# Kernel optimization log

Hardware: AMD Instinct MI355X
Metric: run time of the kernel (lower is better)

The kernel has to match this reference:

```python
import jax, jax.numpy as jnp
import numpy as np

B, D, H, W, Q = 16, 768, 64, 64, 128


def setup_inputs() -> dict:
    key = jax.random.key(0)
    ks = jax.random.split(key, 6)
    s = 0.02  # param init scale
    return {
        "visual_feat": jax.random.normal(ks[0], (B, D, H, W), jnp.float32),
        "text_feat": jax.random.normal(ks[1], (B, Q, D), jnp.float32),
        "Wq": jax.random.normal(ks[2], (D, D), jnp.float32) * s,
        "bq": jnp.zeros((D,), jnp.float32),
        "Wk": jax.random.normal(ks[3], (D, D), jnp.float32) * s,
        "bk": jnp.zeros((D,), jnp.float32),
        "Wv": jax.random.normal(ks[4], (D, D), jnp.float32) * s,
        "bv": jnp.zeros((D,), jnp.float32),
    }


def _entropy_weights(x):
    # x: [B, T, D] -> softmax over features, per-token entropy, softmax over tokens -> [B, T]
    p = jax.nn.softmax(x, axis=-1)
    ent = -jnp.sum(p * jnp.log(p + 1e-9), axis=-1)
    return jax.nn.softmax(ent, axis=-1)


def reference(visual_feat, text_feat, Wq, bq, Wk, bk, Wv, bv):
    b, d, h, w = visual_feat.shape
    vf = visual_feat.reshape(b, d, h * w).transpose(0, 2, 1)  # [B, N, D]
    ve = _entropy_weights(vf)          # [B, N]
    te = _entropy_weights(text_feat)   # [B, Q]
    q = vf @ Wq.T + bq                 # [B, N, D]
    k = text_feat @ Wk.T + bk          # [B, Q, D]
    v = text_feat @ Wv.T + bv          # [B, Q, D]
    attn = jnp.einsum('bnd,bqd->bnq', q, k) / jnp.sqrt(jnp.float32(d))
    attn = attn * (ve[:, :, None] * te[:, None, :])  # entropy outer-product modulation
    attn = jax.nn.softmax(attn, axis=-1)
    enhanced = jnp.einsum('bnq,bqd->bnd', attn, v)   # [B, N, D]
    return enhanced.transpose(0, 2, 1).reshape(b, d, h, w)
```

## Files before the change

kernel.cpp:

```cpp
#include <hip/hip_runtime.h>

#define B_ 16
#define D_ 768
#define N_ 4096
#define Q_ 128

typedef __attribute__((ext_vector_type(4))) float f32x4;
typedef __attribute__((ext_vector_type(8))) short short8;
typedef __attribute__((ext_vector_type(4))) short sv4;

__device__ __forceinline__ unsigned short f2bf(float f) {
  union { float f; unsigned u; } x; x.f = f;
  unsigned u = x.u;
  unsigned r = u + 0x7fffu + ((u >> 16) & 1u);
  return (unsigned short)(r >> 16);
}
__device__ __forceinline__ float bf2f(unsigned short h) {
  union { unsigned u; float f; } x; x.u = ((unsigned)h) << 16;
  return x.f;
}

__global__ __launch_bounds__(256) void cast_bf16_kernel(
    const float* __restrict__ src, unsigned short* __restrict__ dst, int n4) {
  int i = blockIdx.x * 256 + threadIdx.x;
  if (i >= n4) return;
  float4 v = ((const float4*)src)[i];
  ushort4 o;
  o.x = f2bf(v.x); o.y = f2bf(v.y); o.z = f2bf(v.z); o.w = f2bf(v.w);
  ((ushort4*)dst)[i] = o;
}

__global__ __launch_bounds__(256) void transpose_cast_kernel(
    const float* __restrict__ src, unsigned short* __restrict__ dst, int rows, int cols) {
  __shared__ float tile[32][33];
  int bx = blockIdx.x * 32, by = blockIdx.y * 32;
  int tx = threadIdx.x & 31, ty = threadIdx.x >> 5;
  #pragma unroll
  for (int i = 0; i < 32; i += 8)
    tile[ty + i][tx] = src[(size_t)(by + ty + i) * cols + bx + tx];
  __syncthreads();
  #pragma unroll
  for (int i = 0; i < 32; i += 8)
    dst[(size_t)(bx + ty + i) * rows + by + tx] = f2bf(tile[tx][ty + i]);
}

__global__ __launch_bounds__(256) void row_entropy_kernel(
    const float* __restrict__ X, float* __restrict__ ent, int K) {
  int row = blockIdx.x * 4 + (threadIdx.x >> 6);
  int lane = threadIdx.x & 63;
  const float* x = X + (size_t)row * K;
  float m = -__builtin_inff(), s = 0.f, t = 0.f;
  for (int k = lane; k < K; k += 64) {
    float v = x[k];
    float nm = fmaxf(m, v);
    float c = __expf(m - nm);
    float e = __expf(v - nm);
    s = s * c + e;
    t = t * c + v * e;
    m = nm;
  }
  #pragma unroll
  for (int off = 32; off > 0; off >>= 1) {
    float m2 = __shfl_xor(m, off);
    float s2 = __shfl_xor(s, off);
    float t2 = __shfl_xor(t, off);
    float nm = fmaxf(m, m2);
    float c1 = __expf(m - nm), c2 = __expf(m2 - nm);
    s = s * c1 + s2 * c2;
    t = t * c1 + t2 * c2;
    m = nm;
  }
  if (lane == 0) ent[row] = m + __logf(s) - t / s;
}

__global__ __launch_bounds__(256) void visual_entropy_kernel(
    const float* __restrict__ vis, float* __restrict__ ent) {
  int bb = blockIdx.x >> 6;
  int n0 = (blockIdx.x & 63) * 64;
  int t = threadIdx.x;
  int tok = t & 63;
  int slice = t >> 6;
  const float* base = vis + (size_t)bb * D_ * N_ + (size_t)slice * 192 * N_ + n0 + tok;
  float m = -__builtin_inff(), s = 0.f, tt = 0.f;
  for (int d = 0; d < 192; d++) {
    float v = base[(size_t)d * N_];
    float nm = fmaxf(m, v);
    float c = __expf(m - nm);
    float e = __expf(v - nm);
    s = s * c + e; tt = tt * c + v * e; m = nm;
  }
  __shared__ float sm[256], ss[256], st[256];
  sm[t] = m; ss[t] = s; st[t] = tt;
  __syncthreads();
  if (t < 64) {
    #pragma unroll
    for (int k = 1; k < 4; k++) {
      float m2 = sm[t + 64 * k], s2 = ss[t + 64 * k], t2 = st[t + 64 * k];
      float nm = fmaxf(m, m2);
      float c1 = __expf(m - nm), c2 = __expf(m2 - nm);
      s = s * c1 + s2 * c2; tt = tt * c1 + t2 * c2; m = nm;
    }
    ent[(size_t)bb * N_ + n0 + t] = m + __logf(s) - tt / s;
  }
}

__global__ __launch_bounds__(128) void softmax128_kernel(
    const float* __restrict__ ent, float* __restrict__ w) {
  int b = blockIdx.x, t = threadIdx.x;
  float v = ent[b * 128 + t];
  float m = v;
  #pragma unroll
  for (int off = 32; off; off >>= 1) m = fmaxf(m, __shfl_xor(m, off));
  __shared__ float sm2[2], ssum[2];
  int wv = t >> 6;
  if ((t & 63) == 0) sm2[wv] = m;
  __syncthreads();
  m = fmaxf(sm2[0], sm2[1]);
  float e = __expf(v - m);
  float s = e;
  #pragma unroll
  for (int off = 32; off; off >>= 1) s += __shfl_xor(s, off);
  if ((t & 63) == 0) ssum[wv] = s;
  __syncthreads();
  s = ssum[0] + ssum[1];
  w[b * 128 + t] = e / s;
}

__global__ __launch_bounds__(1024) void softmax4096_kernel(
    const float* __restrict__ ent, float* __restrict__ w) {
  int b = blockIdx.x, t = threadIdx.x;
  const float* e = ent + (size_t)b * N_;
  float v[4];
  float m = -__builtin_inff();
  #pragma unroll
  for (int i = 0; i < 4; i++) { v[i] = e[t + 1024 * i]; m = fmaxf(m, v[i]); }
  #pragma unroll
  for (int off = 32; off; off >>= 1) m = fmaxf(m, __shfl_xor(m, off));
  __shared__ float red[16];
  int wv = t >> 6;
  if ((t & 63) == 0) red[wv] = m;
  __syncthreads();
  if (t < 16) {
    float x = red[t];
    #pragma unroll
    for (int off = 8; off; off >>= 1) x = fmaxf(x, __shfl_xor(x, off));
    red[t] = x;
  }
  __syncthreads();
  m = red[0];
  float ev[4];
  float s = 0.f;
  #pragma unroll
  for (int i = 0; i < 4; i++) { ev[i] = __expf(v[i] - m); s += ev[i]; }
  #pragma unroll
  for (int off = 32; off; off >>= 1) s += __shfl_xor(s, off);
  __syncthreads();
  if ((t & 63) == 0) red[wv] = s;
  __syncthreads();
  if (t < 16) {
    float x = red[t];
    #pragma unroll
    for (int off = 8; off; off >>= 1) x += __shfl_xor(x, off);
    red[t] = x;
  }
  __syncthreads();
  s = red[0];
  #pragma unroll
  for (int i = 0; i < 4; i++) w[(size_t)b * N_ + t + 1024 * i] = ev[i] / s;
}

template <int MODE>
__global__ __launch_bounds__(256) void gemm_nt_kernel(
    const unsigned short* __restrict__ A, const unsigned short* __restrict__ Bm,
    const float* __restrict__ bias, unsigned short* __restrict__ C) {
  constexpr int LDA = 40;
  __shared__ unsigned short As[64 * LDA];
  __shared__ unsigned short Bs[64 * LDA];
  int m0 = blockIdx.x * 64, n0 = blockIdx.y * 64;
  int t = threadIdx.x, wave = t >> 6, lane = t & 63;
  int wm = (wave & 1) * 32, wn = (wave >> 1) * 32;
  int fl = lane & 15, fq = lane >> 4;
  f32x4 acc[2][2];
  #pragma unroll
  for (int i = 0; i < 2; i++)
    #pragma unroll
    for (int j = 0; j < 2; j++) acc[i][j] = {0.f, 0.f, 0.f, 0.f};
  int sr = t >> 2, sc = (t & 3) * 8;
  for (int k0 = 0; k0 < D_; k0 += 32) {
    uint4 av = *(const uint4*)(A + (size_t)(m0 + sr) * D_ + k0 + sc);
    uint4 bv = *(const uint4*)(Bm + (size_t)(n0 + sr) * D_ + k0 + sc);
    __syncthreads();
    *(uint4*)(As + sr * LDA + sc) = av;
    *(uint4*)(Bs + sr * LDA + sc) = bv;
    __syncthreads();
    short8 afr[2], bfr[2];
    #pragma unroll
    for (int i = 0; i < 2; i++)
      afr[i] = *(const short8*)(As + (wm + i * 16 + fl) * LDA + fq * 8);
    #pragma unroll
    for (int j = 0; j < 2; j++)
      bfr[j] = *(const short8*)(Bs + (wn + j * 16 + fl) * LDA + fq * 8);
    #pragma unroll
    for (int i = 0; i < 2; i++)
      #pragma unroll
      for (int j = 0; j < 2; j++)
        acc[i][j] = __builtin_amdgcn_mfma_f32_16x16x32_bf16(afr[i], bfr[j], acc[i][j], 0, 0, 0);
  }
  #pragma unroll
  for (int i = 0; i < 2; i++)
    #pragma unroll
    for (int j = 0; j < 2; j++) {
      int n = n0 + wn + j * 16 + fl;
      float bb = (MODE >= 1) ? bias[n] : 0.f;
      #pragma unroll
      for (int r = 0; r < 4; r++) {
        int m = m0 + wm + i * 16 + fq * 4 + r;
        float val = acc[i][j][r] + bb;
        if (MODE == 2) {
          int bt = m >> 7, q = m & 127;
          C[((size_t)bt * D_ + n) * Q_ + q] = f2bf(val);
        } else {
          C[(size_t)m * D_ + n] = f2bf(val);
        }
      }
    }
}

__global__ __launch_bounds__(256) void bias_dot_kernel(
    const unsigned short* __restrict__ kb, const float* __restrict__ bq,
    float* __restrict__ skq) {
  int row = blockIdx.x * 4 + (threadIdx.x >> 6);
  int lane = threadIdx.x & 63;
  const unsigned short* kr = kb + (size_t)row * D_;
  float s = 0.f;
  for (int k = lane; k < D_; k += 64) s += bq[k] * bf2f(kr[k]);
  #pragma unroll
  for (int off = 32; off; off >>= 1) s += __shfl_xor(s, off);
  if (lane == 0) skq[row] = s;
}

__global__ __launch_bounds__(256, 2) void attn_main_kernel(
    const float* __restrict__ vis,
    const unsigned short* __restrict__ kq,
    const unsigned short* __restrict__ vT,
    const float* __restrict__ ve,
    const float* __restrict__ te,
    const float* __restrict__ skq,
    float* __restrict__ out)
{
  constexpr int LA = 68;
  constexpr int LB = 72;
  constexpr int LP = 136;
  __shared__ unsigned short region0[30464];
  __shared__ float stats[2][128][2];
  unsigned short* As = region0;
  unsigned short* Bs = region0 + 8704;
  unsigned short* Ps = region0;
  unsigned short* Vs = region0 + 17408;

  const int bb = blockIdx.x >> 5;
  const int n0 = (blockIdx.x & 31) * 128;
  const int t = threadIdx.x;
  const int wave = t >> 6, lane = t & 63;
  const int fl = lane & 15, fq = lane >> 4;
  const int wm = (wave & 1) * 64;
  const int wq = (wave >> 1) * 64;

  const float* abase = vis + (size_t)bb * D_ * N_ + n0;
  const unsigned short* bbase = kq + (size_t)bb * Q_ * D_;

  f32x4 acc[4][4];
  #pragma unroll
  for (int i = 0; i < 4; i++)
    #pragma unroll
    for (int j = 0; j < 4; j++) acc[i][j] = {0.f, 0.f, 0.f, 0.f};

  const int smi = t & 127;
  const int ph = t >> 7;

  for (int k0 = 0; k0 < D_; k0 += 64) {
    __syncthreads();
    #pragma unroll
    for (int i = 0; i < 16; i++) {
      const int kk = 2 * (ph + 2 * i);
      const float v0 = abase[(size_t)(k0 + kk) * N_ + smi];
      const float v1 = abase[(size_t)(k0 + kk + 1) * N_ + smi];
      const unsigned pk = (unsigned)f2bf(v0) | ((unsigned)f2bf(v1) << 16);
      *(unsigned*)(As + smi * LA + kk) = pk;
    }
    #pragma unroll
    for (int i = 0; i < 4; i++) {
      const int c = t + 256 * i;
      const int q = c >> 3, kc = (c & 7) * 8;
      const uint4 v = *(const uint4*)(bbase + (size_t)q * D_ + k0 + kc);
      *(uint4*)(Bs + q * LB + kc) = v;
    }
    __syncthreads();
    #pragma unroll
    for (int ks = 0; ks < 2; ks++) {
      short8 afr[4], bfr[4];
      #pragma unroll
      for (int i = 0; i < 4; i++) {
        const unsigned short* pa = As + (wm + i * 16 + fl) * LA + ks * 32 + fq * 8;
        sv4 lo = *(const sv4*)pa;
        sv4 hi = *(const sv4*)(pa + 4);
        afr[i] = __builtin_shufflevector(lo, hi, 0, 1, 2, 3, 4, 5, 6, 7);
      }
      #pragma unroll
      for (int j = 0; j < 4; j++)
        bfr[j] = *(const short8*)(Bs + (wq + j * 16 + fl) * LB + ks * 32 + fq * 8);
      #pragma unroll
      for (int i = 0; i < 4; i++)
        #pragma unroll
        for (int j = 0; j < 4; j++)
          acc[i][j] = __builtin_amdgcn_mfma_f32_16x16x32_bf16(afr[i], bfr[j], acc[i][j], 0, 0, 0);
    }
  }

  const float rsD = 0.03608439182435161f;
  float tev[4], skv[4];
  #pragma unroll
  for (int j = 0; j < 4; j++) {
    int q = wq + j * 16 + fl;
    tev[j] = te[bb * Q_ + q];
    skv[j] = skq[bb * Q_ + q];
  }
  float vev4[4][4];
  #pragma unroll
  for (int i = 0; i < 4; i++)
    #pragma unroll
    for (int r = 0; r < 4; r++)
      vev4[i][r] = ve[(size_t)bb * N_ + n0 + wm + i * 16 + fq * 4 + r];

  float rmax[4][4], rsum[4][4];
  #pragma unroll
  for (int i = 0; i < 4; i++)
    #pragma unroll
    for (int r = 0; r < 4; r++) rmax[i][r] = -__builtin_inff();
  #pragma unroll
  for (int i = 0; i < 4; i++)
    #pragma unroll
    for (int j = 0; j < 4; j++)
      #pragma unroll
      for (int r = 0; r < 4; r++) {
        float L = (acc[i][j][r] + skv[j]) * rsD * vev4[i][r] * tev[j];
        acc[i][j][r] = L;
        rmax[i][r] = fmaxf(rmax[i][r], L);
      }
  #pragma unroll
  for (int off = 1; off < 16; off <<= 1)
    #pragma unroll
    for (int i = 0; i < 4; i++)
      #pragma unroll
      for (int r = 0; r < 4; r++)
        rmax[i][r] = fmaxf(rmax[i][r], __shfl_xor(rmax[i][r], off));
  #pragma unroll
  for (int i = 0; i < 4; i++)
    #pragma unroll
    for (int r = 0; r < 4; r++) rsum[i][r] = 0.f;
  #pragma unroll
  for (int i = 0; i < 4; i++)
    #pragma unroll
    for (int j = 0; j < 4; j++)
      #pragma unroll
      for (int r = 0; r < 4; r++) {
        float e = __expf(acc[i][j][r] - rmax[i][r]);
        acc[i][j][r] = e;
        rsum[i][r] += e;
      }
  #pragma unroll
  for (int off = 1; off < 16; off <<= 1)
    #pragma unroll
    for (int i = 0; i < 4; i++)
      #pragma unroll
      for (int r = 0; r < 4; r++) rsum[i][r] += __shfl_xor(rsum[i][r], off);

  const int qh = wq >> 6;
  if (fl == 0) {
    #pragma unroll
    for (int i = 0; i < 4; i++)
      #pragma unroll
      for (int r = 0; r < 4; r++) {
        int m = wm + i * 16 + fq * 4 + r;
        stats[qh][m][0] = rmax[i][r];
        stats[qh][m][1] = rsum[i][r];
      }
  }
  __syncthreads();
  float fac[4][4];
  #pragma unroll
  for (int i = 0; i < 4; i++)
    #pragma unroll
    for (int r = 0; r < 4; r++) {
      int m = wm + i * 16 + fq * 4 + r;
      float M2 = stats[1 - qh][m][0], S2 = stats[1 - qh][m][1];
      float Mf = fmaxf(rmax[i][r], M2);
      float sf = rsum[i][r] * __expf(rmax[i][r] - Mf) + S2 * __expf(M2 - Mf);
      fac[i][r] = __expf(rmax[i][r] - Mf) / sf;
    }
  #pragma unroll
  for (int i = 0; i < 4; i++)
    #pragma unroll
    for (int j = 0; j < 4; j++)
      #pragma unroll
      for (int r = 0; r < 4; r++) {
        int m = wm + i * 16 + fq * 4 + r;
        int q = wq + j * 16 + fl;
        Ps[m * LP + q] = f2bf(acc[i][j][r] * fac[i][r]);
      }

  const int wd = (wave & 1) * 48;
  const int wm2 = (wave >> 1) * 64;
  for (int dc = 0; dc < 8; dc++) {
    __syncthreads();
    const unsigned short* vbase = vT + ((size_t)bb * D_ + dc * 96) * Q_;
    #pragma unroll
    for (int i = 0; i < 6; i++) {
      const int c = t + 256 * i;
      const int d = c >> 4, qc = (c & 15) * 8;
      const uint4 v = *(const uint4*)(vbase + (size_t)d * Q_ + qc);
      *(uint4*)(Vs + d * LP + qc) = v;
    }
    __syncthreads();
    f32x4 acc2[3][4];
    #pragma unroll
    for (int i = 0; i < 3; i++)
      #pragma unroll
      for (int j = 0; j < 4; j++) acc2[i][j] = {0.f, 0.f, 0.f, 0.f};
    #pragma unroll
    for (int ks = 0; ks < 4; ks++) {
      short8 vfr[3], pfr[4];
      #pragma unroll
      for (int i = 0; i < 3; i++)
        vfr[i] = *(const short8*)(Vs + (wd + i * 16 + fl) * LP + ks * 32 + fq * 8);
      #pragma unroll
      for (int j = 0; j < 4; j++)
        pfr[j] = *(const short8*)(Ps + (wm2 + j * 16 + fl) * LP + ks * 32 + fq * 8);
      #pragma unroll
      for (int i = 0; i < 3; i++)
        #pragma unroll
        for (int j = 0; j < 4; j++)
          acc2[i][j] = __builtin_amdgcn_mfma_f32_16x16x32_bf16(vfr[i], pfr[j], acc2[i][j], 0, 0, 0);
    }
    float* obase = out + ((size_t)bb * D_ + dc * 96) * N_ + n0;
    #pragma unroll
    for (int i = 0; i < 3; i++)
      #pragma unroll
      for (int j = 0; j < 4; j++) {
        int mm = wm2 + j * 16 + fl;
        #pragma unroll
        for (int r = 0; r < 4; r++) {
          int d = wd + i * 16 + fq * 4 + r;
          obase[(size_t)d * N_ + mm] = acc2[i][j][r];
        }
      }
  }
}

extern "C" void kernel_launch(void* const* d_in, const int* in_sizes, int n_in,
                              void* d_out, int out_size, void* d_ws, size_t ws_size,
                              hipStream_t stream) {
  const float* vis  = (const float*)d_in[0];
  const float* text = (const float*)d_in[1];
  const float* Wq   = (const float*)d_in[2];
  const float* bq   = (const float*)d_in[3];
  const float* Wk   = (const float*)d_in[4];
  const float* bk   = (const float*)d_in[5];
  const float* Wv   = (const float*)d_in[6];
  const float* bv   = (const float*)d_in[7];
  float* out = (float*)d_out;
  char* ws = (char*)d_ws;

  unsigned short* textb = (unsigned short*)(ws + 0);
  unsigned short* Wkb   = (unsigned short*)(ws + 3145728);
  unsigned short* Wvb   = (unsigned short*)(ws + 4325376);
  unsigned short* WqTb  = (unsigned short*)(ws + 5505024);
  unsigned short* kb    = (unsigned short*)(ws + 6684672);
  unsigned short* kqb   = (unsigned short*)(ws + 9830400);
  unsigned short* vTb   = (unsigned short*)(ws + 12976128);
  float* ent_t = (float*)(ws + 16121856);
  float* tew   = (float*)(ws + 16130048);
  float* ent_v = (float*)(ws + 16138240);
  float* vew   = (float*)(ws + 16400384);
  float* skq   = (float*)(ws + 16662528);

  cast_bf16_kernel<<<1536, 256, 0, stream>>>(text, textb, 2048 * 768 / 4);
  cast_bf16_kernel<<<576, 256, 0, stream>>>(Wk, Wkb, 768 * 768 / 4);
  cast_bf16_kernel<<<576, 256, 0, stream>>>(Wv, Wvb, 768 * 768 / 4);
  transpose_cast_kernel<<<dim3(24, 24), 256, 0, stream>>>(Wq, WqTb, 768, 768);

  row_entropy_kernel<<<512, 256, 0, stream>>>(text, ent_t, 768);
  softmax128_kernel<<<16, 128, 0, stream>>>(ent_t, tew);
  visual_entropy_kernel<<<1024, 256, 0, stream>>>(vis, ent_v);
  softmax4096_kernel<<<16, 1024, 0, stream>>>(ent_v, vew);

  gemm_nt_kernel<1><<<dim3(32, 12), 256, 0, stream>>>(textb, Wkb, bk, kb);
  gemm_nt_kernel<2><<<dim3(32, 12), 256, 0, stream>>>(textb, Wvb, bv, vTb);
  gemm_nt_kernel<0><<<dim3(32, 12), 256, 0, stream>>>(kb, WqTb, nullptr, kqb);
  bias_dot_kernel<<<512, 256, 0, stream>>>(kb, bq, skq);

  attn_main_kernel<<<512, 256, 0, stream>>>(vis, kqb, vTb, vew, tew, skq, out);
}
```

Before: 463.9 us.

## Fuse visual bf16 transpose into entropy pass and async-load attention tiles

The visual entropy kernel now also writes a token-major bf16 copy of the visual features, so the attention kernel can load A tiles with direct global-to-LDS async copies into a swizzled layout instead of doing strided fp32 loads and converting per block. The K·Wq product is reassociated to precompute Wq^T·Wk once, with bias terms folded into vectors u, bw and c0, which removes the dependent k GEMM. This adds roughly 100 MB of extra bf16 write and read traffic, traded against removing the repeated fp32 conversion inside the main kernel.

```diff
diff --git a/kernel.cpp b/kernel.cpp
--- a/kernel.cpp
+++ b/kernel.cpp
@@ -15,9 +15,11 @@
   unsigned r = u + 0x7fffu + ((u >> 16) & 1u);
   return (unsigned short)(r >> 16);
 }
-__device__ __forceinline__ float bf2f(unsigned short h) {
-  union { unsigned u; float f; } x; x.u = ((unsigned)h) << 16;
-  return x.f;
+
+__device__ __forceinline__ void async16(unsigned short* lds, const unsigned short* g) {
+  __builtin_amdgcn_global_load_lds(
+      (const __attribute__((address_space(1))) unsigned int*)g,
+      (__attribute__((address_space(3))) unsigned int*)lds, 16, 0, 0);
 }
 
 __global__ __launch_bounds__(256) void cast_bf16_kernel(
@@ -73,23 +75,38 @@
   if (lane == 0) ent[row] = m + __logf(s) - t / s;
 }
 
-__global__ __launch_bounds__(256) void visual_entropy_kernel(
-    const float* __restrict__ vis, float* __restrict__ ent) {
+__global__ __launch_bounds__(256) void visual_fused_kernel(
+    const float* __restrict__ vis, unsigned short* __restrict__ vfT,
+    float* __restrict__ ent) {
+  constexpr int LT = 72;
+  __shared__ unsigned short tile[64 * LT];
+  __shared__ float sm[256], ss[256], st[256];
   int bb = blockIdx.x >> 6;
   int n0 = (blockIdx.x & 63) * 64;
-  int t = threadIdx.x;
-  int tok = t & 63;
-  int slice = t >> 6;
-  const float* base = vis + (size_t)bb * D_ * N_ + (size_t)slice * 192 * N_ + n0 + tok;
+  int t = threadIdx.x, tok = t & 63, j = t >> 6;
+  const float* base = vis + (size_t)bb * D_ * N_ + n0 + tok;
+  unsigned short* orow = vfT + (size_t)(bb * N_ + n0) * D_;
   float m = -__builtin_inff(), s = 0.f, tt = 0.f;
-  for (int d = 0; d < 192; d++) {
-    float v = base[(size_t)d * N_];
-    float nm = fmaxf(m, v);
-    float c = __expf(m - nm);
-    float e = __expf(v - nm);
-    s = s * c + e; tt = tt * c + v * e; m = nm;
-  }
-  __shared__ float sm[256], ss[256], st[256];
+  for (int dc = 0; dc < 12; dc++) {
+    __syncthreads();
+    #pragma unroll
+    for (int i = 0; i < 16; i++) {
+      int dl = j * 16 + i;
+      float v = base[(size_t)(dc * 64 + dl) * N_];
+      float nm = fmaxf(m, v);
+      float c = __expf(m - nm), e = __expf(v - nm);
+      s = s * c + e; tt = tt * c + v * e; m = nm;
+      tile[tok * LT + dl] = f2bf(v);
+    }
+    __syncthreads();
+    #pragma unroll
+    for (int i2 = 0; i2 < 2; i2++) {
+      int V = i2 * 256 + t;
+      int r = V >> 3, cv = V & 7;
+      short8 pk = *(const short8*)(tile + r * LT + cv * 8);
+      *(short8*)(orow + (size_t)r * D_ + dc * 64 + cv * 8) = pk;
+    }
+  }
   sm[t] = m; ss[t] = s; st[t] = tt;
   __syncthreads();
   if (t < 64) {
@@ -226,21 +243,52 @@
     }
 }
 
-__global__ __launch_bounds__(256) void bias_dot_kernel(
-    const unsigned short* __restrict__ kb, const float* __restrict__ bq,
-    float* __restrict__ skq) {
+__global__ __launch_bounds__(256) void ubw_kernel(
+    const float* __restrict__ Wk, const float* __restrict__ Wq,
+    const float* __restrict__ bq, const float* __restrict__ bk,
+    float* __restrict__ u, float* __restrict__ bw, float* __restrict__ c0) {
+  int blk = blockIdx.x;
+  int t = threadIdx.x;
+  if (blk == 24) {
+    float s = 0.f;
+    for (int d = t; d < D_; d += 256) s += bq[d] * bk[d];
+    #pragma unroll
+    for (int off = 32; off; off >>= 1) s += __shfl_xor(s, off);
+    __shared__ float r4[4];
+    if ((t & 63) == 0) r4[t >> 6] = s;
+    __syncthreads();
+    if (t == 0) c0[0] = r4[0] + r4[1] + r4[2] + r4[3];
+    return;
+  }
+  const float* W = (blk < 12) ? Wk : Wq;
+  const float* bvv = (blk < 12) ? bq : bk;
+  float* outp = (blk < 12) ? u : bw;
+  int e0 = (blk % 12) * 64;
+  int e = e0 + (t & 63), j = t >> 6;
+  float s = 0.f;
+  for (int d = j * 192; d < j * 192 + 192; d++)
+    s += W[(size_t)d * D_ + e] * bvv[d];
+  __shared__ float acc4[4][64];
+  acc4[j][t & 63] = s;
+  __syncthreads();
+  if (t < 64) outp[e0 + t] = acc4[0][t] + acc4[1][t] + acc4[2][t] + acc4[3][t];
+}
+
+__global__ __launch_bounds__(256) void skq_kernel(
+    const float* __restrict__ text, const float* __restrict__ u,
+    const float* __restrict__ c0, float* __restrict__ skq) {
   int row = blockIdx.x * 4 + (threadIdx.x >> 6);
   int lane = threadIdx.x & 63;
-  const unsigned short* kr = kb + (size_t)row * D_;
+  const float* x = text + (size_t)row * D_;
   float s = 0.f;
-  for (int k = lane; k < D_; k += 64) s += bq[k] * bf2f(kr[k]);
+  for (int e = lane; e < D_; e += 64) s += x[e] * u[e];
   #pragma unroll
   for (int off = 32; off; off >>= 1) s += __shfl_xor(s, off);
-  if (lane == 0) skq[row] = s;
+  if (lane == 0) skq[row] = s + c0[0];
 }
 
 __global__ __launch_bounds__(256, 2) void attn_main_kernel(
-    const float* __restrict__ vis,
+    const unsigned short* __restrict__ vfT,
     const unsigned short* __restrict__ kq,
     const unsigned short* __restrict__ vT,
     const float* __restrict__ ve,
@@ -248,13 +296,11 @@
     const float* __restrict__ skq,
     float* __restrict__ out)
 {
-  constexpr int LA = 68;
-  constexpr int LB = 72;
   constexpr int LP = 136;
   __shared__ unsigned short region0[30464];
   __shared__ float stats[2][128][2];
   unsigned short* As = region0;
-  unsigned short* Bs = region0 + 8704;
+  unsigned short* Bs = region0 + 8192;
   unsigned short* Ps = region0;
   unsigned short* Vs = region0 + 17408;
 
@@ -266,8 +312,10 @@
   const int wm = (wave & 1) * 64;
   const int wq = (wave >> 1) * 64;
 
-  const float* abase = vis + (size_t)bb * D_ * N_ + n0;
-  const unsigned short* bbase = kq + (size_t)bb * Q_ * D_;
+  const int rsub = lane >> 3;
+  const int gsw = (lane & 7) ^ rsub;
+  const unsigned short* gA = vfT + (size_t)(bb * N_ + n0 + rsub) * D_ + gsw * 8;
+  const unsigned short* gB = kq + (size_t)(bb * Q_ + rsub) * D_ + gsw * 8;
 
   f32x4 acc[4][4];
   #pragma unroll
@@ -275,40 +323,25 @@
     #pragma unroll
     for (int j = 0; j < 4; j++) acc[i][j] = {0.f, 0.f, 0.f, 0.f};
 
-  const int smi = t & 127;
-  const int ph = t >> 7;
-
   for (int k0 = 0; k0 < D_; k0 += 64) {
     __syncthreads();
     #pragma unroll
-    for (int i = 0; i < 16; i++) {
-      const int kk = 2 * (ph + 2 * i);
-      const float v0 = abase[(size_t)(k0 + kk) * N_ + smi];
-      const float v1 = abase[(size_t)(k0 + kk + 1) * N_ + smi];
-      const unsigned pk = (unsigned)f2bf(v0) | ((unsigned)f2bf(v1) << 16);
-      *(unsigned*)(As + smi * LA + kk) = pk;
-    }
-    #pragma unroll
     for (int i = 0; i < 4; i++) {
-      const int c = t + 256 * i;
-      const int q = c >> 3, kc = (c & 7) * 8;
-      const uint4 v = *(const uint4*)(bbase + (size_t)q * D_ + k0 + kc);
-      *(uint4*)(Bs + q * LB + kc) = v;
+      const int I = wave * 4 + i;
+      async16(As + I * 512, gA + (size_t)I * 8 * D_ + k0);
+      async16(Bs + I * 512, gB + (size_t)I * 8 * D_ + k0);
     }
     __syncthreads();
     #pragma unroll
     for (int ks = 0; ks < 2; ks++) {
       short8 afr[4], bfr[4];
-      #pragma unroll
-      for (int i = 0; i < 4; i++) {
-        const unsigned short* pa = As + (wm + i * 16 + fl) * LA + ks * 32 + fq * 8;
-        sv4 lo = *(const sv4*)pa;
-        sv4 hi = *(const sv4*)(pa + 4);
-        afr[i] = __builtin_shufflevector(lo, hi, 0, 1, 2, 3, 4, 5, 6, 7);
-      }
+      const int p = ((ks * 4 + fq) ^ (fl & 7)) * 8;
+      #pragma unroll
+      for (int i = 0; i < 4; i++)
+        afr[i] = *(const short8*)(As + (wm + i * 16 + fl) * 64 + p);
       #pragma unroll
       for (int j = 0; j < 4; j++)
-        bfr[j] = *(const short8*)(Bs + (wq + j * 16 + fl) * LB + ks * 32 + fq * 8);
+        bfr[j] = *(const short8*)(Bs + (wq + j * 16 + fl) * 64 + p);
       #pragma unroll
       for (int i = 0; i < 4; i++)
         #pragma unroll
@@ -472,32 +505,38 @@
   char* ws = (char*)d_ws;
 
   unsigned short* textb = (unsigned short*)(ws + 0);
-  unsigned short* Wkb   = (unsigned short*)(ws + 3145728);
-  unsigned short* Wvb   = (unsigned short*)(ws + 4325376);
-  unsigned short* WqTb  = (unsigned short*)(ws + 5505024);
-  unsigned short* kb    = (unsigned short*)(ws + 6684672);
-  unsigned short* kqb   = (unsigned short*)(ws + 9830400);
-  unsigned short* vTb   = (unsigned short*)(ws + 12976128);
-  float* ent_t = (float*)(ws + 16121856);
-  float* tew   = (float*)(ws + 16130048);
-  float* ent_v = (float*)(ws + 16138240);
-  float* vew   = (float*)(ws + 16400384);
-  float* skq   = (float*)(ws + 16662528);
+  unsigned short* Wvb   = (unsigned short*)(ws + 3145728);
+  unsigned short* WqTb  = (unsigned short*)(ws + 4325376);
+  unsigned short* WkTb  = (unsigned short*)(ws + 5505024);
+  unsigned short* Wx    = (unsigned short*)(ws + 6684672);
+  unsigned short* kqb   = (unsigned short*)(ws + 7864320);
+  unsigned short* vTb   = (unsigned short*)(ws + 11010048);
+  unsigned short* vfTb  = (unsigned short*)(ws + 14155776);
+  float* ent_t = (float*)(ws + 114819072);
+  float* tew   = (float*)(ws + 114827264);
+  float* ent_v = (float*)(ws + 114835456);
+  float* vew   = (float*)(ws + 115097600);
+  float* skqv  = (float*)(ws + 115359744);
+  float* u     = (float*)(ws + 115367936);
+  float* bw    = (float*)(ws + 115371008);
+  float* c0    = (float*)(ws + 115374080);
 
   cast_bf16_kernel<<<1536, 256, 0, stream>>>(text, textb, 2048 * 768 / 4);
-  cast_bf16_kernel<<<576, 256, 0, stream>>>(Wk, Wkb, 768 * 768 / 4);
   cast_bf16_kernel<<<576, 256, 0, stream>>>(Wv, Wvb, 768 * 768 / 4);
   transpose_cast_kernel<<<dim3(24, 24), 256, 0, stream>>>(Wq, WqTb, 768, 768);
+  transpose_cast_kernel<<<dim3(24, 24), 256, 0, stream>>>(Wk, WkTb, 768, 768);
+
+  gemm_nt_kernel<0><<<dim3(12, 12), 256, 0, stream>>>(WqTb, WkTb, nullptr, Wx);
+  ubw_kernel<<<25, 256, 0, stream>>>(Wk, Wq, bq, bk, u, bw, c0);
+
+  gemm_nt_kernel<1><<<dim3(32, 12), 256, 0, stream>>>(textb, Wx, bw, kqb);
+  gemm_nt_kernel<2><<<dim3(32, 12), 256, 0, stream>>>(textb, Wvb, bv, vTb);
+  skq_kernel<<<512, 256, 0, stream>>>(text, u, c0, skqv);
 
   row_entropy_kernel<<<512, 256, 0, stream>>>(text, ent_t, 768);
   softmax128_kernel<<<16, 128, 0, stream>>>(ent_t, tew);
-  visual_entropy_kernel<<<1024, 256, 0, stream>>>(vis, ent_v);
+  visual_fused_kernel<<<1024, 256, 0, stream>>>(vis, vfTb, ent_v);
   softmax4096_kernel<<<16, 1024, 0, stream>>>(ent_v, vew);
 
-  gemm_nt_kernel<1><<<dim3(32, 12), 256, 0, stream>>>(textb, Wkb, bk, kb);
-  gemm_nt_kernel<2><<<dim3(32, 12), 256, 0, stream>>>(textb, Wvb, bv, vTb);
-  gemm_nt_kernel<0><<<dim3(32, 12), 256, 0, stream>>>(kb, WqTb, nullptr, kqb);
-  bias_dot_kernel<<<512, 256, 0, stream>>>(kb, bq, skq);
-
-  attn_main_kernel<<<512, 256, 0, stream>>>(vis, kqb, vTb, vew, tew, skq, out);
-}
+  attn_main_kernel<<<512, 256, 0, stream>>>(vfTb, kqb, vTb, vew, tew, skqv, out);
+}
```

After: 491.7 us. 6.0% more time.
